# Optimization experiments

Hardware: AMD Instinct MI355X
Metric: run time of the kernel (lower is better)

Reference implementation:

```python
import jax, jax.numpy as jnp
import numpy as np

N = 100000
E = 1600000
IN, HID, OUT = 128, 256, 128


def setup_inputs() -> dict:
    key = jax.random.key(0)
    ks = jax.random.split(key, 12)
    x = jax.random.normal(ks[0], (N, IN), dtype=jnp.float32)
    edge_index = jax.random.randint(ks[1], (2, E), 0, N, dtype=jnp.int64)
    def lin(k, fan_in, fan_out):
        bound = 1.0 / np.sqrt(fan_in)
        return jax.random.uniform(k, (fan_in, fan_out), jnp.float32, -bound, bound)
    return {
        "x": x,
        "edge_index": edge_index,
        # SAGEConv layer 1 (in -> hidden): Wl on aggregated neighbors (with bias), Wr on root
        "Wl1": lin(ks[2], IN, HID), "Wr1": lin(ks[3], IN, HID), "b1": jnp.zeros((HID,), jnp.float32),
        # SAGEConv layer 2 (hidden -> out)
        "Wl2": lin(ks[4], HID, OUT), "Wr2": lin(ks[5], HID, OUT), "b2": jnp.zeros((OUT,), jnp.float32),
        # classifier MLP: out -> hidden -> 2
        "Wc1": lin(ks[6], OUT, HID), "bc1": jnp.zeros((HID,), jnp.float32),
        "Wc2": lin(ks[7], HID, 2), "bc2": jnp.zeros((2,), jnp.float32),
    }


def _sage_conv(x, src, dst, Wl, Wr, b):
    # mean-aggregate neighbor features into dst, then lin_l(agg) + lin_r(x)
    agg = jax.ops.segment_sum(x[src], dst, num_segments=N)          # [N, d]
    cnt = jax.ops.segment_sum(jnp.ones((src.shape[0],), x.dtype), dst, num_segments=N)
    mean = agg / jnp.maximum(cnt, 1.0)[:, None]
    return mean @ Wl + x @ Wr + b


def reference(x, edge_index, Wl1, Wr1, b1, Wl2, Wr2, b2, Wc1, bc1, Wc2, bc2):
    src, dst = edge_index[0], edge_index[1]
    h = jax.nn.relu(_sage_conv(x, src, dst, Wl1, Wr1, b1))  # dropout = identity (eval)
    h = _sage_conv(h, src, dst, Wl2, Wr2, b2)               # node embeddings [N, OUT]
    logits = jax.nn.relu(h @ Wc1 + bc1) @ Wc2 + bc2          # [N, 2]
    return (h, logits)
```

## Files before the change

### kernel.cpp

```cpp
#include <hip/hip_runtime.h>

#define MAXDEG 64
#define BINSHIFT 10
#define CAP 20480
#define CHUNK 4096

typedef __bf16 bf16x8 __attribute__((ext_vector_type(8)));
typedef float f32x4 __attribute__((ext_vector_type(4)));

__device__ inline ushort f2bf(float f) {
    unsigned u = __builtin_bit_cast(unsigned, f);
    return (ushort)((u + 0x7fffu + ((u >> 16) & 1u)) >> 16);
}
__device__ inline float bf2f(ushort h) {
    unsigned u = ((unsigned)h) << 16;
    return __builtin_bit_cast(float, u);
}

__device__ inline void split8(const float* __restrict__ p, bf16x8& hi, bf16x8& lo) {
    float4 v0 = *(const float4*)p;
    float4 v1 = *(const float4*)(p + 4);
    float f[8] = {v0.x, v0.y, v0.z, v0.w, v1.x, v1.y, v1.z, v1.w};
    #pragma unroll
    for (int j = 0; j < 8; ++j) {
        __bf16 h = (__bf16)f[j];
        hi[j] = h;
        lo[j] = (__bf16)(f[j] - (float)h);
    }
}

__global__ __launch_bounds__(256) void bin_edges(
    const int* __restrict__ src, const int* __restrict__ dst,
    int* __restrict__ bincnt, uint2* __restrict__ binbuf, int E)
{
    __shared__ int hist[128];
    __shared__ int base[128];
    const int t = threadIdx.x;
    if (t < 128) hist[t] = 0;
    __syncthreads();

    const int e0 = blockIdx.x * CHUNK;
    int s[16], d[16], sl[16];
    #pragma unroll
    for (int j = 0; j < 16; ++j) {
        int e = e0 + j * 256 + t;
        if (e < E) {
            s[j]  = src[e];
            d[j]  = dst[e];
            sl[j] = atomicAdd(&hist[d[j] >> BINSHIFT], 1);
        } else {
            d[j] = -1;
        }
    }
    __syncthreads();
    if (t < 128 && hist[t] > 0) base[t] = atomicAdd(&bincnt[t], hist[t]);
    __syncthreads();
    #pragma unroll
    for (int j = 0; j < 16; ++j) {
        if (d[j] >= 0) {
            int b = d[j] >> BINSHIFT;
            int pos = base[b] + sl[j];
            if (pos < CAP)
                binbuf[(size_t)b * CAP + pos] = make_uint2((unsigned)s[j], (unsigned)d[j]);
        }
    }
}

__global__ __launch_bounds__(512) void fill_buckets(
    const int* __restrict__ bincnt, const uint2* __restrict__ binbuf,
    int* __restrict__ deg, int* __restrict__ col, int N)
{
    __shared__ int ldeg[1024];
    const int b = blockIdx.x;
    const int t = threadIdx.x;
    ldeg[t] = 0;
    ldeg[t + 512] = 0;
    __syncthreads();
    int cnt = bincnt[b];
    cnt = cnt < CAP ? cnt : CAP;
    const uint2* seg = binbuf + (size_t)b * CAP;
    for (int i = t; i < cnt; i += 512) {
        uint2 e = seg[i];
        int slot = atomicAdd(&ldeg[e.y & 1023], 1);
        if (slot < MAXDEG) col[(size_t)e.y * MAXDEG + slot] = (int)e.x;
    }
    __syncthreads();
    int nb = b << BINSHIFT;
    #pragma unroll
    for (int u = 0; u < 2; ++u) {
        int i = t + u * 512;
        int node = nb + i;
        if (node < N) deg[node] = ldeg[i];
    }
}

__global__ __launch_bounds__(256) void xtobf(
    const float* __restrict__ X, ushort* __restrict__ Xb, int n4)
{
    int i = blockIdx.x * 256 + threadIdx.x;
    if (i >= n4) return;
    float4 v = *(const float4*)(X + (size_t)i * 4);
    *(ushort4*)(Xb + (size_t)i * 4) =
        make_ushort4(f2bf(v.x), f2bf(v.y), f2bf(v.z), f2bf(v.w));
}

__global__ __launch_bounds__(256) void wsplit(
    const float* __restrict__ W, ushort* __restrict__ Thi, ushort* __restrict__ Tlo,
    int K, int N)
{
    int idx = blockIdx.x * 256 + threadIdx.x;
    if (idx >= K * N) return;
    int n = idx / K, k = idx % K;
    float v = W[(size_t)k * N + n];
    ushort h = f2bf(v);
    Thi[idx] = h;
    Tlo[idx] = f2bf(v - bf2f(h));
}

__global__ void make_bcat(const float* __restrict__ b2, float* __restrict__ bcat) {
    int t = threadIdx.x;
    bcat[t] = t < 128 ? 0.f : b2[t - 128];
}

__global__ __launch_bounds__(256) void init_logits(
    const float* __restrict__ bc2, float* __restrict__ out, int M)
{
    int n = blockIdx.x * 256 + threadIdx.x;
    if (n < M) *(float2*)(out + (size_t)n * 2) = make_float2(bc2[0], bc2[1]);
}

__global__ __launch_bounds__(256) void agg_mean_bf16(
    const ushort* __restrict__ Xb, const int* __restrict__ col,
    const int* __restrict__ deg, float* __restrict__ out, int N)
{
    int gw = (blockIdx.x * 256 + threadIdx.x) >> 6;
    if (gw >= N) return;
    int lane = threadIdx.x & 63;
    int sub = lane >> 5;
    int c4  = (lane & 31) * 4;
    int d = deg[gw];
    int dc = d < MAXDEG ? d : MAXDEG;
    const int* cl = col + (size_t)gw * MAXDEG;
    float a0 = 0.f, a1 = 0.f, a2 = 0.f, a3 = 0.f;
    int i = 0;
    for (; i + 8 <= dc; i += 8) {
        int4 id = *(const int4*)(cl + i + sub * 4);
        ushort4 v0 = *(const ushort4*)(Xb + (size_t)id.x * 128 + c4);
        ushort4 v1 = *(const ushort4*)(Xb + (size_t)id.y * 128 + c4);
        ushort4 v2 = *(const ushort4*)(Xb + (size_t)id.z * 128 + c4);
        ushort4 v3 = *(const ushort4*)(Xb + (size_t)id.w * 128 + c4);
        a0 += (bf2f(v0.x) + bf2f(v1.x)) + (bf2f(v2.x) + bf2f(v3.x));
        a1 += (bf2f(v0.y) + bf2f(v1.y)) + (bf2f(v2.y) + bf2f(v3.y));
        a2 += (bf2f(v0.z) + bf2f(v1.z)) + (bf2f(v2.z) + bf2f(v3.z));
        a3 += (bf2f(v0.w) + bf2f(v1.w)) + (bf2f(v2.w) + bf2f(v3.w));
    }
    for (; i < dc; i += 2) {
        int j = i + sub;
        if (j < dc) {
            ushort4 v = *(const ushort4*)(Xb + (size_t)cl[j] * 128 + c4);
            a0 += bf2f(v.x); a1 += bf2f(v.y); a2 += bf2f(v.z); a3 += bf2f(v.w);
        }
    }
    a0 += __shfl_xor(a0, 32); a1 += __shfl_xor(a1, 32);
    a2 += __shfl_xor(a2, 32); a3 += __shfl_xor(a3, 32);
    if (sub == 0) {
        float inv = 1.0f / (float)(d > 1 ? d : 1);
        *(float4*)(out + (size_t)gw * 128 + c4) =
            make_float4(a0 * inv, a1 * inv, a2 * inv, a3 * inv);
    }
}

__global__ __launch_bounds__(256) void agg_finish(
    const ushort* __restrict__ t2b, const float* __restrict__ tcat2,
    const int* __restrict__ col, const int* __restrict__ deg,
    float* __restrict__ h2, int N)
{
    int gw = (blockIdx.x * 256 + threadIdx.x) >> 6;
    if (gw >= N) return;
    int lane = threadIdx.x & 63;
    int sub = lane >> 5;
    int c4  = (lane & 31) * 4;
    int d = deg[gw];
    int dc = d < MAXDEG ? d : MAXDEG;
    const int* cl = col + (size_t)gw * MAXDEG;
    float a0 = 0.f, a1 = 0.f, a2 = 0.f, a3 = 0.f;
    int i = 0;
    for (; i + 8 <= dc; i += 8) {
        int4 id = *(const int4*)(cl + i + sub * 4);
        ushort4 v0 = *(const ushort4*)(t2b + (size_t)id.x * 128 + c4);
        ushort4 v1 = *(const ushort4*)(t2b + (size_t)id.y * 128 + c4);
        ushort4 v2 = *(const ushort4*)(t2b + (size_t)id.z * 128 + c4);
        ushort4 v3 = *(const ushort4*)(t2b + (size_t)id.w * 128 + c4);
        a0 += (bf2f(v0.x) + bf2f(v1.x)) + (bf2f(v2.x) + bf2f(v3.x));
        a1 += (bf2f(v0.y) + bf2f(v1.y)) + (bf2f(v2.y) + bf2f(v3.y));
        a2 += (bf2f(v0.z) + bf2f(v1.z)) + (bf2f(v2.z) + bf2f(v3.z));
        a3 += (bf2f(v0.w) + bf2f(v1.w)) + (bf2f(v2.w) + bf2f(v3.w));
    }
    for (; i < dc; i += 2) {
        int j = i + sub;
        if (j < dc) {
            ushort4 v = *(const ushort4*)(t2b + (size_t)cl[j] * 128 + c4);
            a0 += bf2f(v.x); a1 += bf2f(v.y); a2 += bf2f(v.z); a3 += bf2f(v.w);
        }
    }
    a0 += __shfl_xor(a0, 32); a1 += __shfl_xor(a1, 32);
    a2 += __shfl_xor(a2, 32); a3 += __shfl_xor(a3, 32);
    if (sub == 0) {
        float inv = 1.0f / (float)(d > 1 ? d : 1);
        float4 hp = *(const float4*)(tcat2 + (size_t)gw * 128 + c4);
        *(float4*)(h2 + (size_t)gw * 128 + c4) = make_float4(
            a0 * inv + hp.x, a1 * inv + hp.y, a2 * inv + hp.z, a3 * inv + hp.w);
    }
}

template<int K, int NPH, int MODE>
__global__ __launch_bounds__(512, 4) void gemm_tile(
    const float* __restrict__ A1, const float* __restrict__ A2,
    const ushort* __restrict__ B1hi, const ushort* __restrict__ B1lo,
    const ushort* __restrict__ B2hi, const ushort* __restrict__ B2lo,
    const float* __restrict__ bias, const float* __restrict__ Wc2,
    float* __restrict__ outf, ushort* __restrict__ outt2, int M, int relu)
{
    __shared__ __align__(16) ushort Ah[128 * 40];
    __shared__ __align__(16) ushort Al[128 * 40];
    __shared__ __align__(16) ushort BhS[128 * 40];
    __shared__ __align__(16) ushort BlS[128 * 40];
    __shared__ float sw0[MODE == 1 ? 256 : 4], sw1[MODE == 1 ? 256 : 4];

    const int t = threadIdx.x;
    if constexpr (MODE == 1) {
        if (t < 256) {
            sw0[t] = Wc2[t * 2 + 0];
            sw1[t] = Wc2[t * 2 + 1];
        }
    }

    const int m0 = blockIdx.x * 128;
    const int n0 = blockIdx.y * 128;
    const int l  = t & 63;
    const int wv = t >> 6;
    const int wr = (wv >> 1) * 32;
    const int wc = (wv & 1) * 64;
    const int lr = l & 15;
    const int kb = l >> 4;

    const int sr = t >> 2;
    const int sq = t & 3;

    f32x4 acc[2][4] = {};

    #pragma unroll
    for (int ph = 0; ph < NPH; ++ph) {
        const float*  A  = ph ? A2 : A1;
        const ushort* Bh = ph ? B2hi : B1hi;
        const ushort* Bl = ph ? B2lo : B1lo;
        for (int k0 = 0; k0 < K; k0 += 32) {
            __syncthreads();
            {
                int rg = m0 + sr;
                rg = rg < M ? rg : M - 1;
                const float* p = A + (size_t)rg * K + k0 + sq * 8;
                bf16x8 h0, l0;
                split8(p, h0, l0);
                int base = sr * 40 + sq * 8;
                *(bf16x8*)&Ah[base] = h0;
                *(bf16x8*)&Al[base] = l0;
            }
            {
                const ushort* ph_ = Bh + (size_t)(n0 + sr) * K + k0 + sq * 8;
                const ushort* pl_ = Bl + (size_t)(n0 + sr) * K + k0 + sq * 8;
                int base = sr * 40 + sq * 8;
                *(uint4*)&BhS[base] = *(const uint4*)ph_;
                *(uint4*)&BlS[base] = *(const uint4*)pl_;
            }
            __syncthreads();
            bf16x8 ah[2], al_[2];
            #pragma unroll
            for (int mi = 0; mi < 2; ++mi) {
                int off = (wr + mi * 16 + lr) * 40 + kb * 8;
                ah[mi]  = *(const bf16x8*)&Ah[off];
                al_[mi] = *(const bf16x8*)&Al[off];
            }
            #pragma unroll
            for (int nj = 0; nj < 4; ++nj) {
                int off = (wc + nj * 16 + lr) * 40 + kb * 8;
                bf16x8 bh = *(const bf16x8*)&BhS[off];
                bf16x8 bl = *(const bf16x8*)&BlS[off];
                #pragma unroll
                for (int mi = 0; mi < 2; ++mi) {
                    acc[mi][nj] = __builtin_amdgcn_mfma_f32_16x16x32_bf16(ah[mi],  bh, acc[mi][nj], 0, 0, 0);
                    acc[mi][nj] = __builtin_amdgcn_mfma_f32_16x16x32_bf16(al_[mi], bh, acc[mi][nj], 0, 0, 0);
                    acc[mi][nj] = __builtin_amdgcn_mfma_f32_16x16x32_bf16(ah[mi],  bl, acc[mi][nj], 0, 0, 0);
                }
            }
        }
    }

    if constexpr (MODE != 1) {
        #pragma unroll
        for (int nj = 0; nj < 4; ++nj) {
            int lc   = wc + nj * 16 + lr;
            int colg = n0 + lc;
            float bv = bias[colg];
            #pragma unroll
            for (int mi = 0; mi < 2; ++mi) {
                #pragma unroll
                for (int reg = 0; reg < 4; ++reg) {
                    int rowg = m0 + wr + mi * 16 + kb * 4 + reg;
                    if (rowg >= M) continue;
                    float v = acc[mi][nj][reg] + bv;
                    if (relu) v = fmaxf(v, 0.f);
                    if constexpr (MODE == 0) {
                        outf[(size_t)rowg * 256 + colg] = v;
                    } else {
                        if (n0 == 0) outt2[(size_t)rowg * 128 + lc] = f2bf(v);
                        else         outf[(size_t)rowg * 128 + lc] = v;
                    }
                }
            }
        }
    } else {
        #pragma unroll
        for (int mi = 0; mi < 2; ++mi) {
            #pragma unroll
            for (int reg = 0; reg < 4; ++reg) {
                float s0 = 0.f, s1 = 0.f;
                #pragma unroll
                for (int nj = 0; nj < 4; ++nj) {
                    int colg = n0 + wc + nj * 16 + lr;
                    float v = fmaxf(acc[mi][nj][reg] + bias[colg], 0.f);
                    s0 += v * sw0[colg];
                    s1 += v * sw1[colg];
                }
                #pragma unroll
                for (int mk = 1; mk < 16; mk <<= 1) {
                    s0 += __shfl_xor(s0, mk);
                    s1 += __shfl_xor(s1, mk);
                }
                int rowg = m0 + wr + mi * 16 + kb * 4 + reg;
                if (lr == 0 && rowg < M) {
                    atomicAdd(&outf[(size_t)rowg * 2 + 0], s0);
                    atomicAdd(&outf[(size_t)rowg * 2 + 1], s1);
                }
            }
        }
    }
}

extern "C" void kernel_launch(void* const* d_in, const int* in_sizes, int n_in,
                              void* d_out, int out_size, void* d_ws, size_t ws_size,
                              hipStream_t stream)
{
    const float* x   = (const float*)d_in[0];
    const int*   ei  = (const int*)d_in[1];
    const float* Wl1 = (const float*)d_in[2];
    const float* Wr1 = (const float*)d_in[3];
    const float* b1  = (const float*)d_in[4];
    const float* Wl2 = (const float*)d_in[5];
    const float* Wr2 = (const float*)d_in[6];
    const float* b2  = (const float*)d_in[7];
    const float* Wc1 = (const float*)d_in[8];
    const float* bc1 = (const float*)d_in[9];
    const float* Wc2 = (const float*)d_in[10];
    const float* bc2 = (const float*)d_in[11];

    const int N = in_sizes[0] / 128;
    const int E = in_sizes[1] / 2;
    const int nbins = (N + (1 << BINSHIFT) - 1) >> BINSHIFT;

    char* ws = (char*)d_ws;
    size_t off = 0;
    auto alloc = [&](size_t bytes) -> void* {
        void* p = ws + off;
        off += (bytes + 255) & ~(size_t)255;
        return p;
    };
    const size_t NE128 = (size_t)N * 128;
    const size_t NE256 = (size_t)N * 256;

    int*    bincnt = (int*)alloc((size_t)nbins * 4);
    int*    deg  = (int*)alloc((size_t)N * 4);
    int*    colb = (int*)alloc((size_t)N * MAXDEG * 4);
    char*   bufA = (char*)alloc(NE256 * 4);
    char*   bufB = (char*)alloc(NE256 * 4);
    ushort* wl1h = (ushort*)alloc(256 * 128 * 2); ushort* wl1l = (ushort*)alloc(256 * 128 * 2);
    ushort* wr1h = (ushort*)alloc(256 * 128 * 2); ushort* wr1l = (ushort*)alloc(256 * 128 * 2);
    ushort* w2h  = (ushort*)alloc(256 * 256 * 2); ushort* w2l  = (ushort*)alloc(256 * 256 * 2);
    ushort* wc1h = (ushort*)alloc(256 * 128 * 2); ushort* wc1l = (ushort*)alloc(256 * 128 * 2);
    float*  bcat = (float*)alloc(256 * 4);

    uint2*  binbuf = (uint2*)bufA;
    float*  a1    = (float*)bufA;
    ushort* t2b   = (ushort*)bufA;
    float*  tcat2 = (float*)(bufA + NE128 * 2);
    ushort* xb    = (ushort*)bufB;
    float*  h1    = (float*)bufB;

    float* h2     = (float*)d_out;
    float* logits = (float*)d_out + NE128;

    const int gm = (N + 127) / 128;

    hipMemsetAsync(bincnt, 0, (size_t)nbins * 4, stream);

    bin_edges<<<dim3((E + CHUNK - 1) / CHUNK), dim3(256), 0, stream>>>(
        ei, ei + E, bincnt, binbuf, E);
    fill_buckets<<<dim3(nbins), dim3(512), 0, stream>>>(bincnt, binbuf, deg, colb, N);

    xtobf<<<dim3((int)(NE128 / 4 + 255) / 256), dim3(256), 0, stream>>>(x, xb, (int)(NE128 / 4));
    wsplit<<<dim3(128), dim3(256), 0, stream>>>(Wl1, wl1h, wl1l, 128, 256);
    wsplit<<<dim3(128), dim3(256), 0, stream>>>(Wr1, wr1h, wr1l, 128, 256);
    wsplit<<<dim3(128), dim3(256), 0, stream>>>(Wl2, w2h, w2l, 256, 128);
    wsplit<<<dim3(128), dim3(256), 0, stream>>>(Wr2, w2h + 128 * 256, w2l + 128 * 256, 256, 128);
    wsplit<<<dim3(128), dim3(256), 0, stream>>>(Wc1, wc1h, wc1l, 128, 256);
    make_bcat<<<dim3(1), dim3(256), 0, stream>>>(b2, bcat);
    init_logits<<<dim3((N + 255) / 256), dim3(256), 0, stream>>>(bc2, logits, N);

    agg_mean_bf16<<<dim3((N + 3) / 4), dim3(256), 0, stream>>>(xb, colb, deg, a1, N);
    gemm_tile<128, 2, 0><<<dim3(gm, 2), dim3(512), 0, stream>>>(
        a1, x, wl1h, wl1l, wr1h, wr1l, b1, nullptr, h1, nullptr, N, 1);

    gemm_tile<256, 1, 3><<<dim3(gm, 2), dim3(512), 0, stream>>>(
        h1, nullptr, w2h, w2l, nullptr, nullptr, bcat, nullptr, tcat2, t2b, N, 0);

    agg_finish<<<dim3((N + 3) / 4), dim3(256), 0, stream>>>(
        t2b, tcat2, colb, deg, h2, N);

    gemm_tile<128, 1, 1><<<dim3(gm, 2), dim3(512), 0, stream>>>(
        h2, nullptr, wc1h, wc1l, nullptr, nullptr, bc1, Wc2, logits, nullptr, N, 1);
}
```

Measured before the change: 407.6 us.

## Use finer edge bins, fuse prep kernels, and unroll gather loops 16-wide

Shrinks destination bins from 1024 to 256 nodes so fill_buckets launches about four times as many blocks, improving parallelism in the CSR build. Merges the bf16 conversion, weight splitting, bias concat and logits init into a single prep kernel to cut launch overhead. Adds a 16-neighbor unrolled loop in both aggregation kernels for more outstanding loads. The smaller per-bin capacity leaves less slack, so a bin overflowing its capacity would silently drop edges.

```diff
diff --git a/kernel.cpp b/kernel.cpp
--- a/kernel.cpp
+++ b/kernel.cpp
@@ -1,8 +1,8 @@
 #include <hip/hip_runtime.h>
 
 #define MAXDEG 64
-#define BINSHIFT 10
-#define CAP 20480
+#define BINSHIFT 8
+#define CAP 5120
 #define CHUNK 4096
 
 typedef __bf16 bf16x8 __attribute__((ext_vector_type(8)));
@@ -31,12 +31,13 @@
 
 __global__ __launch_bounds__(256) void bin_edges(
     const int* __restrict__ src, const int* __restrict__ dst,
-    int* __restrict__ bincnt, uint2* __restrict__ binbuf, int E)
-{
-    __shared__ int hist[128];
-    __shared__ int base[128];
+    int* __restrict__ bincnt, uint2* __restrict__ binbuf, int E, int nbins)
+{
+    __shared__ int hist[512];
+    __shared__ int base[512];
     const int t = threadIdx.x;
-    if (t < 128) hist[t] = 0;
+    hist[t] = 0;
+    hist[t + 256] = 0;
     __syncthreads();
 
     const int e0 = blockIdx.x * CHUNK;
@@ -53,7 +54,8 @@
         }
     }
     __syncthreads();
-    if (t < 128 && hist[t] > 0) base[t] = atomicAdd(&bincnt[t], hist[t]);
+    for (int b = t; b < nbins; b += 256)
+        if (hist[b] > 0) base[b] = atomicAdd(&bincnt[b], hist[b]);
     __syncthreads();
     #pragma unroll
     for (int j = 0; j < 16; ++j) {
@@ -70,63 +72,73 @@
     const int* __restrict__ bincnt, const uint2* __restrict__ binbuf,
     int* __restrict__ deg, int* __restrict__ col, int N)
 {
-    __shared__ int ldeg[1024];
+    __shared__ int ldeg[256];
     const int b = blockIdx.x;
     const int t = threadIdx.x;
-    ldeg[t] = 0;
-    ldeg[t + 512] = 0;
+    if (t < 256) ldeg[t] = 0;
     __syncthreads();
     int cnt = bincnt[b];
     cnt = cnt < CAP ? cnt : CAP;
     const uint2* seg = binbuf + (size_t)b * CAP;
     for (int i = t; i < cnt; i += 512) {
         uint2 e = seg[i];
-        int slot = atomicAdd(&ldeg[e.y & 1023], 1);
+        int slot = atomicAdd(&ldeg[e.y & 255], 1);
         if (slot < MAXDEG) col[(size_t)e.y * MAXDEG + slot] = (int)e.x;
     }
     __syncthreads();
-    int nb = b << BINSHIFT;
-    #pragma unroll
-    for (int u = 0; u < 2; ++u) {
-        int i = t + u * 512;
-        int node = nb + i;
-        if (node < N) deg[node] = ldeg[i];
-    }
-}
-
-__global__ __launch_bounds__(256) void xtobf(
-    const float* __restrict__ X, ushort* __restrict__ Xb, int n4)
-{
-    int i = blockIdx.x * 256 + threadIdx.x;
-    if (i >= n4) return;
-    float4 v = *(const float4*)(X + (size_t)i * 4);
-    *(ushort4*)(Xb + (size_t)i * 4) =
-        make_ushort4(f2bf(v.x), f2bf(v.y), f2bf(v.z), f2bf(v.w));
-}
-
-__global__ __launch_bounds__(256) void wsplit(
-    const float* __restrict__ W, ushort* __restrict__ Thi, ushort* __restrict__ Tlo,
-    int K, int N)
-{
-    int idx = blockIdx.x * 256 + threadIdx.x;
-    if (idx >= K * N) return;
-    int n = idx / K, k = idx % K;
-    float v = W[(size_t)k * N + n];
-    ushort h = f2bf(v);
-    Thi[idx] = h;
-    Tlo[idx] = f2bf(v - bf2f(h));
-}
-
-__global__ void make_bcat(const float* __restrict__ b2, float* __restrict__ bcat) {
-    int t = threadIdx.x;
+    if (t < 256) {
+        int node = (b << BINSHIFT) + t;
+        if (node < N) deg[node] = ldeg[t];
+    }
+}
+
+__global__ __launch_bounds__(256) void prep_all(
+    const float* __restrict__ x, ushort* __restrict__ xb, int n4, int nxb,
+    const float* __restrict__ Wl1, ushort* __restrict__ wl1h, ushort* __restrict__ wl1l,
+    const float* __restrict__ Wr1, ushort* __restrict__ wr1h, ushort* __restrict__ wr1l,
+    const float* __restrict__ Wl2, const float* __restrict__ Wr2,
+    ushort* __restrict__ w2h, ushort* __restrict__ w2l,
+    const float* __restrict__ Wc1, ushort* __restrict__ wc1h, ushort* __restrict__ wc1l,
+    const float* __restrict__ b2, float* __restrict__ bcat,
+    const float* __restrict__ bc2, float* __restrict__ logits, int N, int nlb)
+{
+    const int bid = blockIdx.x;
+    const int t = threadIdx.x;
+    if (bid < nxb) {
+        int i = bid * 256 + t;
+        if (i < n4) {
+            float4 v = *(const float4*)(x + (size_t)i * 4);
+            *(ushort4*)(xb + (size_t)i * 4) =
+                make_ushort4(f2bf(v.x), f2bf(v.y), f2bf(v.z), f2bf(v.w));
+        }
+        return;
+    }
+    int wb = bid - nxb;
+    if (wb < 640) {
+        int w = wb >> 7;
+        int idx = (wb & 127) * 256 + t;
+        const float* W; ushort* Th; ushort* Tl; int K, Nn;
+        switch (w) {
+            case 0: W = Wl1; Th = wl1h; Tl = wl1l; K = 128; Nn = 256; break;
+            case 1: W = Wr1; Th = wr1h; Tl = wr1l; K = 128; Nn = 256; break;
+            case 2: W = Wl2; Th = w2h;  Tl = w2l;  K = 256; Nn = 128; break;
+            case 3: W = Wr2; Th = w2h + 128 * 256; Tl = w2l + 128 * 256; K = 256; Nn = 128; break;
+            default: W = Wc1; Th = wc1h; Tl = wc1l; K = 128; Nn = 256; break;
+        }
+        int n = idx / K, k = idx % K;
+        float v = W[(size_t)k * Nn + n];
+        ushort h = f2bf(v);
+        Th[idx] = h;
+        Tl[idx] = f2bf(v - bf2f(h));
+        return;
+    }
+    wb -= 640;
+    if (wb < nlb) {
+        int n = wb * 256 + t;
+        if (n < N) *(float2*)(logits + (size_t)n * 2) = make_float2(bc2[0], bc2[1]);
+        return;
+    }
     bcat[t] = t < 128 ? 0.f : b2[t - 128];
-}
-
-__global__ __launch_bounds__(256) void init_logits(
-    const float* __restrict__ bc2, float* __restrict__ out, int M)
-{
-    int n = blockIdx.x * 256 + threadIdx.x;
-    if (n < M) *(float2*)(out + (size_t)n * 2) = make_float2(bc2[0], bc2[1]);
 }
 
 __global__ __launch_bounds__(256) void agg_mean_bf16(
@@ -143,6 +155,26 @@
     const int* cl = col + (size_t)gw * MAXDEG;
     float a0 = 0.f, a1 = 0.f, a2 = 0.f, a3 = 0.f;
     int i = 0;
+    for (; i + 16 <= dc; i += 16) {
+        int4 ida = *(const int4*)(cl + i + sub * 4);
+        int4 idb = *(const int4*)(cl + i + 8 + sub * 4);
+        ushort4 v0 = *(const ushort4*)(Xb + (size_t)ida.x * 128 + c4);
+        ushort4 v1 = *(const ushort4*)(Xb + (size_t)ida.y * 128 + c4);
+        ushort4 v2 = *(const ushort4*)(Xb + (size_t)ida.z * 128 + c4);
+        ushort4 v3 = *(const ushort4*)(Xb + (size_t)ida.w * 128 + c4);
+        ushort4 v4 = *(const ushort4*)(Xb + (size_t)idb.x * 128 + c4);
+        ushort4 v5 = *(const ushort4*)(Xb + (size_t)idb.y * 128 + c4);
+        ushort4 v6 = *(const ushort4*)(Xb + (size_t)idb.z * 128 + c4);
+        ushort4 v7 = *(const ushort4*)(Xb + (size_t)idb.w * 128 + c4);
+        a0 += ((bf2f(v0.x) + bf2f(v1.x)) + (bf2f(v2.x) + bf2f(v3.x)))
+            + ((bf2f(v4.x) + bf2f(v5.x)) + (bf2f(v6.x) + bf2f(v7.x)));
+        a1 += ((bf2f(v0.y) + bf2f(v1.y)) + (bf2f(v2.y) + bf2f(v3.y)))
+            + ((bf2f(v4.y) + bf2f(v5.y)) + (bf2f(v6.y) + bf2f(v7.y)));
+        a2 += ((bf2f(v0.z) + bf2f(v1.z)) + (bf2f(v2.z) + bf2f(v3.z)))
+            + ((bf2f(v4.z) + bf2f(v5.z)) + (bf2f(v6.z) + bf2f(v7.z)));
+        a3 += ((bf2f(v0.w) + bf2f(v1.w)) + (bf2f(v2.w) + bf2f(v3.w)))
+            + ((bf2f(v4.w) + bf2f(v5.w)) + (bf2f(v6.w) + bf2f(v7.w)));
+    }
     for (; i + 8 <= dc; i += 8) {
         int4 id = *(const int4*)(cl + i + sub * 4);
         ushort4 v0 = *(const ushort4*)(Xb + (size_t)id.x * 128 + c4);
@@ -185,6 +217,26 @@
     const int* cl = col + (size_t)gw * MAXDEG;
     float a0 = 0.f, a1 = 0.f, a2 = 0.f, a3 = 0.f;
     int i = 0;
+    for (; i + 16 <= dc; i += 16) {
+        int4 ida = *(const int4*)(cl + i + sub * 4);
+        int4 idb = *(const int4*)(cl + i + 8 + sub * 4);
+        ushort4 v0 = *(const ushort4*)(t2b + (size_t)ida.x * 128 + c4);
+        ushort4 v1 = *(const ushort4*)(t2b + (size_t)ida.y * 128 + c4);
+        ushort4 v2 = *(const ushort4*)(t2b + (size_t)ida.z * 128 + c4);
+        ushort4 v3 = *(const ushort4*)(t2b + (size_t)ida.w * 128 + c4);
+        ushort4 v4 = *(const ushort4*)(t2b + (size_t)idb.x * 128 + c4);
+        ushort4 v5 = *(const ushort4*)(t2b + (size_t)idb.y * 128 + c4);
+        ushort4 v6 = *(const ushort4*)(t2b + (size_t)idb.z * 128 + c4);
+        ushort4 v7 = *(const ushort4*)(t2b + (size_t)idb.w * 128 + c4);
+        a0 += ((bf2f(v0.x) + bf2f(v1.x)) + (bf2f(v2.x) + bf2f(v3.x)))
+            + ((bf2f(v4.x) + bf2f(v5.x)) + (bf2f(v6.x) + bf2f(v7.x)));
+        a1 += ((bf2f(v0.y) + bf2f(v1.y)) + (bf2f(v2.y) + bf2f(v3.y)))
+            + ((bf2f(v4.y) + bf2f(v5.y)) + (bf2f(v6.y) + bf2f(v7.y)));
+        a2 += ((bf2f(v0.z) + bf2f(v1.z)) + (bf2f(v2.z) + bf2f(v3.z)))
+            + ((bf2f(v4.z) + bf2f(v5.z)) + (bf2f(v6.z) + bf2f(v7.z)));
+        a3 += ((bf2f(v0.w) + bf2f(v1.w)) + (bf2f(v2.w) + bf2f(v3.w)))
+            + ((bf2f(v4.w) + bf2f(v5.w)) + (bf2f(v6.w) + bf2f(v7.w)));
+    }
     for (; i + 8 <= dc; i += 8) {
         int4 id = *(const int4*)(cl + i + sub * 4);
         ushort4 v0 = *(const ushort4*)(t2b + (size_t)id.x * 128 + c4);
@@ -399,22 +451,22 @@
     float* h2     = (float*)d_out;
     float* logits = (float*)d_out + NE128;
 
-    const int gm = (N + 127) / 128;
+    const int gm  = (N + 127) / 128;
+    const int n4  = (int)(NE128 / 4);
+    const int nxb = (n4 + 255) / 256;
+    const int nlb = (N + 255) / 256;
 
     hipMemsetAsync(bincnt, 0, (size_t)nbins * 4, stream);
 
     bin_edges<<<dim3((E + CHUNK - 1) / CHUNK), dim3(256), 0, stream>>>(
-        ei, ei + E, bincnt, binbuf, E);
+        ei, ei + E, bincnt, binbuf, E, nbins);
     fill_buckets<<<dim3(nbins), dim3(512), 0, stream>>>(bincnt, binbuf, deg, colb, N);
 
-    xtobf<<<dim3((int)(NE128 / 4 + 255) / 256), dim3(256), 0, stream>>>(x, xb, (int)(NE128 / 4));
-    wsplit<<<dim3(128), dim3(256), 0, stream>>>(Wl1, wl1h, wl1l, 128, 256);
-    wsplit<<<dim3(128), dim3(256), 0, stream>>>(Wr1, wr1h, wr1l, 128, 256);
-    wsplit<<<dim3(128), dim3(256), 0, stream>>>(Wl2, w2h, w2l, 256, 128);
-    wsplit<<<dim3(128), dim3(256), 0, stream>>>(Wr2, w2h + 128 * 256, w2l + 128 * 256, 256, 128);
-    wsplit<<<dim3(128), dim3(256), 0, stream>>>(Wc1, wc1h, wc1l, 128, 256);
-    make_bcat<<<dim3(1), dim3(256), 0, stream>>>(b2, bcat);
-    init_logits<<<dim3((N + 255) / 256), dim3(256), 0, stream>>>(bc2, logits, N);
+    prep_all<<<dim3(nxb + 640 + nlb + 1), dim3(256), 0, stream>>>(
+        x, xb, n4, nxb,
+        Wl1, wl1h, wl1l, Wr1, wr1h, wr1l,
+        Wl2, Wr2, w2h, w2l, Wc1, wc1h, wc1l,
+        b2, bcat, bc2, logits, N, nlb);
 
     agg_mean_bf16<<<dim3((N + 3) / 4), dim3(256), 0, stream>>>(xb, colb, deg, a1, N);
     gemm_tile<128, 2, 0><<<dim3(gm, 2), dim3(512), 0, stream>>>(
```

Measured after the change: 383.6 us. -5.9%, faster.
